# Optimization experiments

Measured on AMD Instinct MI355X. Metric: run time of the kernel, lower is better.

The kernel has to match this reference:

```python
import jax, jax.numpy as jnp
import numpy as np

N = 100000   # nodes
E = 1600000  # edges
IN = 64      # in_channels
H = 128      # hidden_features
G = 1024     # graphs in batch
NUM_REST = 3 # num_layers (extra GraphConv layers)


def setup_inputs() -> dict:
    key = jax.random.key(0)
    ks = jax.random.split(key, 12)
    x = jax.random.normal(ks[0], (N, IN), jnp.float32)
    edge_index = jax.random.randint(ks[1], (2, E), 0, N)
    edge_attr = jax.random.uniform(ks[2], (E,), jnp.float32)
    batch = jnp.sort(jax.random.randint(ks[3], (N,), 0, G))

    def glorot(k, shape, fan_in):
        return jax.random.normal(k, shape, jnp.float32) / np.float32(np.sqrt(fan_in))

    # GraphConv layer 0: in -> hidden (lin_root: no bias, lin_rel: bias)
    W_root0 = glorot(ks[4], (H, IN), IN)
    W_rel0 = glorot(ks[5], (H, IN), IN)
    b0 = jnp.zeros((H,), jnp.float32)
    # GraphConv layers 1..3: hidden -> hidden (stacked)
    W_root_r = glorot(ks[6], (NUM_REST, H, H), H)
    W_rel_r = glorot(ks[7], (NUM_REST, H, H), H)
    b_r = jnp.zeros((NUM_REST, H), jnp.float32)
    # MLPReadout: [H -> H//2 -> 1]
    Wr1 = glorot(ks[8], (H // 2, H), H)
    br1 = jnp.zeros((H // 2,), jnp.float32)
    Wr2 = glorot(ks[9], (1, H // 2), H // 2)
    br2 = jnp.zeros((1,), jnp.float32)
    return dict(x=x, edge_index=edge_index, edge_attr=edge_attr, batch=batch,
                W_root0=W_root0, W_rel0=W_rel0, b0=b0,
                W_root_r=W_root_r, W_rel_r=W_rel_r, b_r=b_r,
                Wr1=Wr1, br1=br1, Wr2=Wr2, br2=br2)


def graph_conv(x, src, dst, ew, W_root, W_rel, b):
    # PyG GraphConv (aggr='add'):
    #   out_i = W_rel @ sum_{j->i} e_ji * x_j + b + W_root @ x_i
    msg = ew[:, None] * x[src]                                   # [E, d]
    agg = jax.ops.segment_sum(msg, dst, num_segments=x.shape[0])  # [N, d]
    return agg @ W_rel.T + b + x @ W_root.T


def reference(x, edge_index, edge_attr, batch,
              W_root0, W_rel0, b0, W_root_r, W_rel_r, b_r,
              Wr1, br1, Wr2, br2):
    src, dst = edge_index[0], edge_index[1]
    y = graph_conv(x, src, dst, edge_attr, W_root0, W_rel0, b0)
    for l in range(W_root_r.shape[0]):
        y = graph_conv(y, src, dst, edge_attr, W_root_r[l], W_rel_r[l], b_r[l])
    # MLPReadout: Linear -> ReLU -> Linear
    y = jax.nn.relu(y @ Wr1.T + br1)
    y = y @ Wr2.T + br2                                           # [N, 1]
    # scatter-mean over graph assignment
    num = jax.ops.segment_sum(y, batch, num_segments=G)           # [G, 1]
    cnt = jax.ops.segment_sum(jnp.ones((y.shape[0], 1), y.dtype), batch,
                              num_segments=G)
    return num / jnp.maximum(cnt, 1.0)                            # [G, 1]
```

## Files before the change

kernel.cpp:

```cpp
#include <hip/hip_runtime.h>
#include <hip/hip_fp16.h>
#include <cstdint>
#include <cstddef>

#define NNODES 100000
#define NEDGES 1600000
#define NGRAPH 1024

#define BK 256
#define NBUCKET 391
#define CHUNK 4096
#define NCHUNK 391
#define NBE (NBUCKET * NCHUNK)

typedef __attribute__((ext_vector_type(8))) short short8;
typedef __attribute__((ext_vector_type(8))) unsigned short ushort8;
typedef __attribute__((ext_vector_type(4))) float f32x4;

__device__ inline float b2f(unsigned short u) {
  return __uint_as_float(((unsigned int)u) << 16);
}
__device__ inline unsigned short f2b(float f) {
  unsigned int x = __float_as_uint(f);
  x += 0x7fffu + ((x >> 16) & 1u);
  return (unsigned short)(x >> 16);
}
__device__ inline unsigned int pack_edge(int src, float w) {
  unsigned short hb = __half_as_ushort(__float2half_rn(w));
  return ((unsigned int)src << 15) | ((unsigned int)hb >> 1);
}
__device__ inline void unpack_edge(unsigned int p, int& src, float& w) {
  src = (int)(p >> 15);
  w = __half2float(__ushort_as_half((unsigned short)((p & 0x7fffu) << 1)));
}

__global__ __launch_bounds__(256) void prepack_kernel(
    const float* __restrict__ Wrel0, const float* __restrict__ Wroot0,
    const float* __restrict__ WrelR, const float* __restrict__ WrootR,
    const float* __restrict__ Wr1, unsigned short* __restrict__ dst)
{
  int g = blockIdx.x * 256 + threadIdx.x;
  if (g >= 15360) return;
  const float* src; int H, K, r; unsigned short* out;
  if (g < 1024)       { src = Wrel0;  H = 128; K = 64;  r = g;        out = dst + r * 8; }
  else if (g < 2048)  { src = Wroot0; H = 128; K = 64;  r = g - 1024; out = dst + 8192 + r * 8; }
  else if (g < 8192)  { int m = g - 2048; int l = m / 2048; r = m % 2048;
                        src = WrelR + l * 16384;  H = 128; K = 128;
                        out = dst + 16384 + l * 16384 + r * 8; }
  else if (g < 14336) { int m = g - 8192; int l = m / 2048; r = m % 2048;
                        src = WrootR + l * 16384; H = 128; K = 128;
                        out = dst + 65536 + l * 16384 + r * 8; }
  else                { src = Wr1;    H = 64;  K = 128; r = g - 14336; out = dst + 114688 + r * 8; }
  int n = r % H, k8 = r / H;
  const float* s = src + (size_t)n * K + k8 * 8;
#pragma unroll
  for (int j = 0; j < 8; j++) out[j] = f2b(s[j]);
}

__global__ __launch_bounds__(256) void cvt_x_kernel(
    const float* __restrict__ x, unsigned short* __restrict__ xb)
{
  int i = blockIdx.x * 256 + threadIdx.x;
  if (i * 4 >= NNODES * 64) return;
  float4 v = *(const float4*)(x + i * 4);
  ushort4 o;
  o.x = f2b(v.x); o.y = f2b(v.y); o.z = f2b(v.z); o.w = f2b(v.w);
  *(ushort4*)(xb + i * 4) = o;
}

__global__ __launch_bounds__(256) void bucket_count_kernel(
    const int* __restrict__ ei, int* __restrict__ cnt)
{
  __shared__ int hist[NBUCKET];
  for (int i = threadIdx.x; i < NBUCKET; i += 256) hist[i] = 0;
  __syncthreads();
  int base = blockIdx.x * CHUNK;
  for (int t = threadIdx.x; t < CHUNK; t += 256) {
    int e = base + t;
    if (e < NEDGES) atomicAdd(&hist[ei[NEDGES + e] >> 8], 1);
  }
  __syncthreads();
  for (int i = threadIdx.x; i < NBUCKET; i += 256)
    cnt[i * NCHUNK + blockIdx.x] = hist[i];
}

__global__ __launch_bounds__(512) void row_scan_kernel(
    int* __restrict__ cnt, int* __restrict__ rowsum)
{
  __shared__ int s[512];
  int b = blockIdx.x, t = threadIdx.x;
  int v = (t < NCHUNK) ? cnt[b * NCHUNK + t] : 0;
  s[t] = v;
  __syncthreads();
#pragma unroll
  for (int off = 1; off < 512; off <<= 1) {
    int u = (t >= off) ? s[t - off] : 0;
    __syncthreads();
    s[t] += u;
    __syncthreads();
  }
  if (t < NCHUNK) cnt[b * NCHUNK + t] = s[t] - v;
  if (t == 511) rowsum[b] = s[511];
}

__global__ __launch_bounds__(512) void rowbase_scan_kernel(
    const int* __restrict__ rowsum, int* __restrict__ rowbase)
{
  __shared__ int s[512];
  int t = threadIdx.x;
  int v = (t < NBUCKET) ? rowsum[t] : 0;
  s[t] = v;
  __syncthreads();
#pragma unroll
  for (int off = 1; off < 512; off <<= 1) {
    int u = (t >= off) ? s[t - off] : 0;
    __syncthreads();
    s[t] += u;
    __syncthreads();
  }
  if (t < NBUCKET) rowbase[t] = s[t] - v;
  if (t == 511) rowbase[NBUCKET] = s[511];
}

__global__ __launch_bounds__(256) void bucket_scatter_kernel(
    const int* __restrict__ ei, const float* __restrict__ ew,
    const int* __restrict__ cnt, const int* __restrict__ rowbase,
    uint2* __restrict__ rec)
{
  __shared__ int pos[NBUCKET];
  for (int i = threadIdx.x; i < NBUCKET; i += 256)
    pos[i] = rowbase[i] + cnt[i * NCHUNK + blockIdx.x];
  __syncthreads();
  int base = blockIdx.x * CHUNK;
  for (int t = threadIdx.x; t < CHUNK; t += 256) {
    int e = base + t;
    if (e < NEDGES) {
      int d = ei[NEDGES + e];
      int p = atomicAdd(&pos[d >> 8], 1);
      rec[p] = make_uint2((unsigned int)d, pack_edge(ei[e], ew[e]));
    }
  }
}

__global__ __launch_bounds__(256) void bucket_fill_kernel(
    const int* __restrict__ rowbase, const uint2* __restrict__ rec,
    unsigned int* __restrict__ epack, int* __restrict__ row_ptr)
{
  __shared__ int off[BK];
  __shared__ int s[256];
  int b = blockIdx.x, t = threadIdx.x;
  int start = rowbase[b];
  int end = rowbase[b + 1];
  int nbase = b * BK;
  off[t] = 0;
  __syncthreads();
  for (int i = start + t; i < end; i += 256)
    atomicAdd(&off[rec[i].x - nbase], 1);
  __syncthreads();
  int v = off[t];
  s[t] = v;
  __syncthreads();
#pragma unroll
  for (int o = 1; o < 256; o <<= 1) {
    int u = (t >= o) ? s[t - o] : 0;
    __syncthreads();
    s[t] += u;
    __syncthreads();
  }
  int ex = s[t] - v;
  int g = nbase + t;
  if (g <= NNODES) row_ptr[g] = start + ex;
  __syncthreads();
  off[t] = ex;
  __syncthreads();
  for (int i = start + t; i < end; i += 256) {
    uint2 r = rec[i];
    int lp = atomicAdd(&off[r.x - nbase], 1);
    epack[start + lp] = r.y;
  }
}

__global__ __launch_bounds__(256) void gptr_kernel(
    const int* __restrict__ batch, int* __restrict__ gptr)
{
  int i = blockIdx.x * 256 + threadIdx.x;
  if (i >= NNODES) return;
  int b = batch[i];
  int bn = (i + 1 < NNODES) ? batch[i + 1] : NGRAPH;
  for (int g = b + 1; g <= bn; g++) gptr[g] = i + 1;
  if (i == 0) for (int g = 0; g <= b; g++) gptr[g] = 0;
}

__global__ __launch_bounds__(256) void agg128_kernel(
    const int* __restrict__ row_ptr, const unsigned int* __restrict__ epack,
    const unsigned short* __restrict__ x, unsigned short* __restrict__ agg)
{
  int node = blockIdx.x * 4 + (threadIdx.x >> 6);
  int lane = threadIdx.x & 63;
  if (node >= NNODES) return;
  int q = lane >> 4, sl = lane & 15;
  int s = row_ptr[node], e = row_ptr[node + 1];
  float acc[8];
#pragma unroll
  for (int j = 0; j < 8; j++) acc[j] = 0.f;

  for (int i = s + q; i < e; i += 16) {
    unsigned int p0 = epack[i];
    unsigned int p1 = (i + 4  < e) ? epack[i + 4]  : 0u;
    unsigned int p2 = (i + 8  < e) ? epack[i + 8]  : 0u;
    unsigned int p3 = (i + 12 < e) ? epack[i + 12] : 0u;
    int s0, s1, s2, s3; float w0, w1, w2, w3;
    unpack_edge(p0, s0, w0);
    unpack_edge(p1, s1, w1);
    unpack_edge(p2, s2, w2);
    unpack_edge(p3, s3, w3);
    ushort8 r0 = *(const ushort8*)(x + (size_t)s0 * 128 + sl * 8);
    ushort8 r1 = *(const ushort8*)(x + (size_t)s1 * 128 + sl * 8);
    ushort8 r2 = *(const ushort8*)(x + (size_t)s2 * 128 + sl * 8);
    ushort8 r3 = *(const ushort8*)(x + (size_t)s3 * 128 + sl * 8);
#pragma unroll
    for (int j = 0; j < 8; j++)
      acc[j] += w0 * b2f(r0[j]) + w1 * b2f(r1[j]) +
                w2 * b2f(r2[j]) + w3 * b2f(r3[j]);
  }
#pragma unroll
  for (int j = 0; j < 8; j++) {
    acc[j] += __shfl_xor(acc[j], 16, 64);
    acc[j] += __shfl_xor(acc[j], 32, 64);
  }
  if (q == 0) {
    ushort8 o;
#pragma unroll
    for (int j = 0; j < 8; j++) o[j] = f2b(acc[j]);
    *(ushort8*)(agg + (size_t)node * 128 + sl * 8) = o;
  }
}

__global__ __launch_bounds__(256) void agg64_kernel(
    const int* __restrict__ row_ptr, const unsigned int* __restrict__ epack,
    const unsigned short* __restrict__ x, unsigned short* __restrict__ agg)
{
  int node = blockIdx.x * 4 + (threadIdx.x >> 6);
  int lane = threadIdx.x & 63;
  if (node >= NNODES) return;
  int q = lane >> 3, sl = lane & 7;
  int s = row_ptr[node], e = row_ptr[node + 1];
  float acc[8];
#pragma unroll
  for (int j = 0; j < 8; j++) acc[j] = 0.f;

  for (int i = s + q; i < e; i += 16) {
    unsigned int p0 = epack[i];
    unsigned int p1 = (i + 8 < e) ? epack[i + 8] : 0u;
    int s0, s1; float w0, w1;
    unpack_edge(p0, s0, w0);
    unpack_edge(p1, s1, w1);
    ushort8 r0 = *(const ushort8*)(x + (size_t)s0 * 64 + sl * 8);
    ushort8 r1 = *(const ushort8*)(x + (size_t)s1 * 64 + sl * 8);
#pragma unroll
    for (int j = 0; j < 8; j++)
      acc[j] += w0 * b2f(r0[j]) + w1 * b2f(r1[j]);
  }
#pragma unroll
  for (int j = 0; j < 8; j++) {
    acc[j] += __shfl_xor(acc[j], 8, 64);
    acc[j] += __shfl_xor(acc[j], 16, 64);
    acc[j] += __shfl_xor(acc[j], 32, 64);
  }
  if (q == 0) {
    ushort8 o;
#pragma unroll
    for (int j = 0; j < 8; j++) o[j] = f2b(acc[j]);
    *(ushort8*)(agg + (size_t)node * 64 + sl * 8) = o;
  }
}

template <int KDIM, int HOUT, int MT, bool DUAL, bool RELU>
__global__ __launch_bounds__(256) void mfma_gemm(
    const unsigned short* __restrict__ A1, const unsigned short* __restrict__ W1,
    const unsigned short* __restrict__ A2, const unsigned short* __restrict__ W2,
    const float* __restrict__ bias, unsigned short* __restrict__ out)
{
  constexpr int NT2 = HOUT / 16;
  constexpr int KC = KDIM / 32;
  const int wave = threadIdx.x >> 6, lane = threadIdx.x & 63;
  const int quad = lane >> 4, l16 = lane & 15;
  const int n0 = (blockIdx.x * 4 + wave) * (MT * 16);

  f32x4 acc[MT][NT2];
#pragma unroll
  for (int m = 0; m < MT; m++)
#pragma unroll
    for (int t = 0; t < NT2; t++) acc[m][t] = (f32x4){0.f, 0.f, 0.f, 0.f};

  int nodes[MT];
#pragma unroll
  for (int m = 0; m < MT; m++) {
    int nd = n0 + m * 16 + l16;
    nodes[m] = nd < NNODES ? nd : NNODES - 1;
  }

#pragma unroll
  for (int c = 0; c < KC; c++) {
    short8 bfr[NT2];
#pragma unroll
    for (int t = 0; t < NT2; t++)
      bfr[t] = *(const short8*)(W1 + ((size_t)(c * 4 + quad) * HOUT + t * 16 + l16) * 8);
#pragma unroll
    for (int m = 0; m < MT; m++) {
      short8 af = *(const short8*)(A1 + (size_t)nodes[m] * KDIM + c * 32 + quad * 8);
#pragma unroll
      for (int t = 0; t < NT2; t++)
        acc[m][t] = __builtin_amdgcn_mfma_f32_16x16x32_bf16(af, bfr[t], acc[m][t], 0, 0, 0);
    }
    if (DUAL) {
#pragma unroll
      for (int t = 0; t < NT2; t++)
        bfr[t] = *(const short8*)(W2 + ((size_t)(c * 4 + quad) * HOUT + t * 16 + l16) * 8);
#pragma unroll
      for (int m = 0; m < MT; m++) {
        short8 af = *(const short8*)(A2 + (size_t)nodes[m] * KDIM + c * 32 + quad * 8);
#pragma unroll
        for (int t = 0; t < NT2; t++)
          acc[m][t] = __builtin_amdgcn_mfma_f32_16x16x32_bf16(af, bfr[t], acc[m][t], 0, 0, 0);
      }
    }
  }

#pragma unroll
  for (int m = 0; m < MT; m++) {
    int rowbase = n0 + m * 16 + quad * 4;
#pragma unroll
    for (int t = 0; t < NT2; t++) {
      float b = bias[t * 16 + l16];
#pragma unroll
      for (int r = 0; r < 4; r++) {
        int nd = rowbase + r;
        if (nd < NNODES) {
          float v = acc[m][t][r] + b;
          if (RELU) v = fmaxf(v, 0.f);
          out[(size_t)nd * HOUT + t * 16 + l16] = f2b(v);
        }
      }
    }
  }
}

__global__ __launch_bounds__(256) void readout_reduce_kernel(
    const unsigned short* __restrict__ h, const float* __restrict__ Wr2,
    const float* __restrict__ br2, const int* __restrict__ gptr,
    float* __restrict__ out)
{
  __shared__ float wsum[4];
  int g = blockIdx.x;
  int s = gptr[g], e = gptr[g + 1];
  int wave = threadIdx.x >> 6, lane = threadIdx.x & 63;
  float w2 = Wr2[lane];
  float acc = 0.f;
  for (int n = s + wave; n < e; n += 4)
    acc += b2f(h[(size_t)n * 64 + lane]) * w2;
#pragma unroll
  for (int off = 32; off >= 1; off >>= 1) acc += __shfl_xor(acc, off, 64);
  if (lane == 0) wsum[wave] = acc;
  __syncthreads();
  if (threadIdx.x == 0) {
    float cnt = (float)(e - s);
    float sum = wsum[0] + wsum[1] + wsum[2] + wsum[3] + cnt * br2[0];
    out[g] = sum / fmaxf(cnt, 1.f);
  }
}

extern "C" void kernel_launch(void* const* d_in, const int* in_sizes, int n_in,
                              void* d_out, int out_size, void* d_ws, size_t ws_size,
                              hipStream_t stream)
{
  const float* x      = (const float*)d_in[0];
  const int*   ei     = (const int*)d_in[1];
  const float* ew     = (const float*)d_in[2];
  const int*   batch  = (const int*)d_in[3];
  const float* Wroot0 = (const float*)d_in[4];
  const float* Wrel0  = (const float*)d_in[5];
  const float* b0     = (const float*)d_in[6];
  const float* WrootR = (const float*)d_in[7];
  const float* WrelR  = (const float*)d_in[8];
  const float* bR     = (const float*)d_in[9];
  const float* Wr1    = (const float*)d_in[10];
  const float* br1    = (const float*)d_in[11];
  const float* Wr2    = (const float*)d_in[12];
  const float* br2    = (const float*)d_in[13];

  char* ws = (char*)d_ws;
  unsigned short* wp   = (unsigned short*)ws;
  unsigned short* xb   = wp + 131072;
  unsigned short* agg0 = xb + (size_t)NNODES * 64;
  unsigned short* bufA = agg0 + (size_t)NNODES * 64;
  unsigned short* bufB = bufA + (size_t)NNODES * 128;
  unsigned short* hbuf = bufB + (size_t)NNODES * 128;
  int*  cnt      = (int*)(hbuf + (size_t)NNODES * 64);
  int*  rowsum   = cnt + ((NBE + 63) & ~63);
  int*  rowbase  = rowsum + NBUCKET + 1;
  int*  row_ptr  = rowbase + NBUCKET + 1;
  int*  gptr     = row_ptr + NNODES + 2;
  unsigned int* epack = (unsigned int*)(gptr + NGRAPH + 2);
  uint2* rec = (uint2*)bufA;

  prepack_kernel<<<60, 256, 0, stream>>>(Wrel0, Wroot0, WrelR, WrootR, Wr1, wp);
  cvt_x_kernel<<<(NNODES * 64 / 4 + 255) / 256, 256, 0, stream>>>(x, xb);

  const unsigned short* pWrel0  = wp;
  const unsigned short* pWroot0 = wp + 8192;
  const unsigned short* pWrelR  = wp + 16384;
  const unsigned short* pWrootR = wp + 65536;
  const unsigned short* pWr1    = wp + 114688;

  bucket_count_kernel<<<NCHUNK, 256, 0, stream>>>(ei, cnt);
  row_scan_kernel<<<NBUCKET, 512, 0, stream>>>(cnt, rowsum);
  rowbase_scan_kernel<<<1, 512, 0, stream>>>(rowsum, rowbase);
  bucket_scatter_kernel<<<NCHUNK, 256, 0, stream>>>(ei, ew, cnt, rowbase, rec);
  bucket_fill_kernel<<<NBUCKET, 256, 0, stream>>>(rowbase, rec, epack, row_ptr);
  gptr_kernel<<<(NNODES + 255) / 256, 256, 0, stream>>>(batch, gptr);

  agg64_kernel<<<(NNODES + 3) / 4, 256, 0, stream>>>(row_ptr, epack, xb, agg0);
  mfma_gemm<64, 128, 2, true, false><<<(NNODES + 127) / 128, 256, 0, stream>>>(
      agg0, pWrel0, xb, pWroot0, b0, bufB);

  unsigned short* bufs[2] = { bufB, bufA };
  for (int l = 0; l < 3; l++) {
    unsigned short* in  = bufs[l & 1];
    unsigned short* agg = bufs[(l & 1) ^ 1];
    agg128_kernel<<<(NNODES + 3) / 4, 256, 0, stream>>>(row_ptr, epack, in, agg);
    mfma_gemm<128, 128, 2, true, false><<<(NNODES + 127) / 128, 256, 0, stream>>>(
        agg, pWrelR + l * 16384, in, pWrootR + l * 16384, bR + l * 128, agg);
  }

  mfma_gemm<128, 64, 4, false, true><<<(NNODES + 255) / 256, 256, 0, stream>>>(
      bufA, pWr1, nullptr, nullptr, br1, hbuf);
  readout_reduce_kernel<<<NGRAPH, 256, 0, stream>>>(hbuf, Wr2, br2, gptr, (float*)d_out);
}
```

Baseline: 506.1 us.

## Fuse neighbor aggregation and dual GEMM into one per-tile layer kernel

Replaces the separate aggregation kernel and dual-input MFMA GEMM with one kernel per layer. Each 64-node tile gathers its neighbor sums into swizzled LDS, then runs the rel/root MFMA GEMMs from LDS and global input. This drops the global write and re-read of the aggregate buffer and one launch per layer. The cost is larger blocks with more serial per-wave work (16 nodes per wave, processed one after another), which may reduce latency hiding for the gather. Output is written as scalar 2-byte stores.

```diff
diff --git a/kernel.cpp b/kernel.cpp
--- a/kernel.cpp
+++ b/kernel.cpp
@@ -191,87 +191,130 @@
   if (i == 0) for (int g = 0; g <= b; g++) gptr[g] = 0;
 }
 
-__global__ __launch_bounds__(256) void agg128_kernel(
+template <int KDIM>
+__global__ __launch_bounds__(256) void fused_layer(
     const int* __restrict__ row_ptr, const unsigned int* __restrict__ epack,
-    const unsigned short* __restrict__ x, unsigned short* __restrict__ agg)
-{
-  int node = blockIdx.x * 4 + (threadIdx.x >> 6);
-  int lane = threadIdx.x & 63;
-  if (node >= NNODES) return;
-  int q = lane >> 4, sl = lane & 15;
-  int s = row_ptr[node], e = row_ptr[node + 1];
-  float acc[8];
-#pragma unroll
-  for (int j = 0; j < 8; j++) acc[j] = 0.f;
-
-  for (int i = s + q; i < e; i += 16) {
-    unsigned int p0 = epack[i];
-    unsigned int p1 = (i + 4  < e) ? epack[i + 4]  : 0u;
-    unsigned int p2 = (i + 8  < e) ? epack[i + 8]  : 0u;
-    unsigned int p3 = (i + 12 < e) ? epack[i + 12] : 0u;
-    int s0, s1, s2, s3; float w0, w1, w2, w3;
-    unpack_edge(p0, s0, w0);
-    unpack_edge(p1, s1, w1);
-    unpack_edge(p2, s2, w2);
-    unpack_edge(p3, s3, w3);
-    ushort8 r0 = *(const ushort8*)(x + (size_t)s0 * 128 + sl * 8);
-    ushort8 r1 = *(const ushort8*)(x + (size_t)s1 * 128 + sl * 8);
-    ushort8 r2 = *(const ushort8*)(x + (size_t)s2 * 128 + sl * 8);
-    ushort8 r3 = *(const ushort8*)(x + (size_t)s3 * 128 + sl * 8);
-#pragma unroll
-    for (int j = 0; j < 8; j++)
-      acc[j] += w0 * b2f(r0[j]) + w1 * b2f(r1[j]) +
-                w2 * b2f(r2[j]) + w3 * b2f(r3[j]);
-  }
-#pragma unroll
-  for (int j = 0; j < 8; j++) {
-    acc[j] += __shfl_xor(acc[j], 16, 64);
-    acc[j] += __shfl_xor(acc[j], 32, 64);
-  }
-  if (q == 0) {
-    ushort8 o;
-#pragma unroll
-    for (int j = 0; j < 8; j++) o[j] = f2b(acc[j]);
-    *(ushort8*)(agg + (size_t)node * 128 + sl * 8) = o;
-  }
-}
-
-__global__ __launch_bounds__(256) void agg64_kernel(
-    const int* __restrict__ row_ptr, const unsigned int* __restrict__ epack,
-    const unsigned short* __restrict__ x, unsigned short* __restrict__ agg)
-{
-  int node = blockIdx.x * 4 + (threadIdx.x >> 6);
-  int lane = threadIdx.x & 63;
-  if (node >= NNODES) return;
-  int q = lane >> 3, sl = lane & 7;
-  int s = row_ptr[node], e = row_ptr[node + 1];
-  float acc[8];
-#pragma unroll
-  for (int j = 0; j < 8; j++) acc[j] = 0.f;
-
-  for (int i = s + q; i < e; i += 16) {
-    unsigned int p0 = epack[i];
-    unsigned int p1 = (i + 8 < e) ? epack[i + 8] : 0u;
-    int s0, s1; float w0, w1;
-    unpack_edge(p0, s0, w0);
-    unpack_edge(p1, s1, w1);
-    ushort8 r0 = *(const ushort8*)(x + (size_t)s0 * 64 + sl * 8);
-    ushort8 r1 = *(const ushort8*)(x + (size_t)s1 * 64 + sl * 8);
-#pragma unroll
-    for (int j = 0; j < 8; j++)
-      acc[j] += w0 * b2f(r0[j]) + w1 * b2f(r1[j]);
-  }
-#pragma unroll
-  for (int j = 0; j < 8; j++) {
-    acc[j] += __shfl_xor(acc[j], 8, 64);
-    acc[j] += __shfl_xor(acc[j], 16, 64);
-    acc[j] += __shfl_xor(acc[j], 32, 64);
-  }
-  if (q == 0) {
-    ushort8 o;
-#pragma unroll
-    for (int j = 0; j < 8; j++) o[j] = f2b(acc[j]);
-    *(ushort8*)(agg + (size_t)node * 64 + sl * 8) = o;
+    const unsigned short* __restrict__ in,
+    const unsigned short* __restrict__ W1, const unsigned short* __restrict__ W2,
+    const float* __restrict__ bias, unsigned short* __restrict__ out)
+{
+  constexpr int ROWB = KDIM * 2;
+  __shared__ __align__(16) unsigned char lds[64 * ROWB];
+  const int wave = threadIdx.x >> 6, lane = threadIdx.x & 63;
+  const int tile0 = blockIdx.x * 64;
+
+  {
+    int q, sl;
+    if (KDIM == 128) { q = lane >> 4; sl = lane & 15; }
+    else             { q = lane >> 3; sl = lane & 7;  }
+    for (int nn = 0; nn < 16; nn++) {
+      int lrow = wave * 16 + nn;
+      int node = tile0 + lrow;
+      float acc[8];
+#pragma unroll
+      for (int j = 0; j < 8; j++) acc[j] = 0.f;
+      if (node < NNODES) {
+        int s = row_ptr[node], e = row_ptr[node + 1];
+        if (KDIM == 128) {
+          for (int i = s + q; i < e; i += 16) {
+            unsigned int p0 = epack[i];
+            unsigned int p1 = (i + 4  < e) ? epack[i + 4]  : 0u;
+            unsigned int p2 = (i + 8  < e) ? epack[i + 8]  : 0u;
+            unsigned int p3 = (i + 12 < e) ? epack[i + 12] : 0u;
+            int s0, s1, s2, s3; float w0, w1, w2, w3;
+            unpack_edge(p0, s0, w0);
+            unpack_edge(p1, s1, w1);
+            unpack_edge(p2, s2, w2);
+            unpack_edge(p3, s3, w3);
+            ushort8 r0 = *(const ushort8*)(in + (size_t)s0 * 128 + sl * 8);
+            ushort8 r1 = *(const ushort8*)(in + (size_t)s1 * 128 + sl * 8);
+            ushort8 r2 = *(const ushort8*)(in + (size_t)s2 * 128 + sl * 8);
+            ushort8 r3 = *(const ushort8*)(in + (size_t)s3 * 128 + sl * 8);
+#pragma unroll
+            for (int j = 0; j < 8; j++)
+              acc[j] += w0 * b2f(r0[j]) + w1 * b2f(r1[j]) +
+                        w2 * b2f(r2[j]) + w3 * b2f(r3[j]);
+          }
+#pragma unroll
+          for (int j = 0; j < 8; j++) {
+            acc[j] += __shfl_xor(acc[j], 16, 64);
+            acc[j] += __shfl_xor(acc[j], 32, 64);
+          }
+        } else {
+          for (int i = s + q; i < e; i += 16) {
+            unsigned int p0 = epack[i];
+            unsigned int p1 = (i + 8 < e) ? epack[i + 8] : 0u;
+            int s0, s1; float w0, w1;
+            unpack_edge(p0, s0, w0);
+            unpack_edge(p1, s1, w1);
+            ushort8 r0 = *(const ushort8*)(in + (size_t)s0 * 64 + sl * 8);
+            ushort8 r1 = *(const ushort8*)(in + (size_t)s1 * 64 + sl * 8);
+#pragma unroll
+            for (int j = 0; j < 8; j++)
+              acc[j] += w0 * b2f(r0[j]) + w1 * b2f(r1[j]);
+          }
+#pragma unroll
+          for (int j = 0; j < 8; j++) {
+            acc[j] += __shfl_xor(acc[j], 8, 64);
+            acc[j] += __shfl_xor(acc[j], 16, 64);
+            acc[j] += __shfl_xor(acc[j], 32, 64);
+          }
+        }
+      }
+      if (q == 0) {
+        ushort8 o;
+#pragma unroll
+        for (int j = 0; j < 8; j++) o[j] = f2b(acc[j]);
+        int boff = lrow * ROWB + ((sl * 16) ^ ((lrow & 7) << 4));
+        *(ushort8*)(lds + boff) = o;
+      }
+    }
+  }
+  __syncthreads();
+
+  constexpr int NT2 = 8;
+  constexpr int KC = KDIM / 32;
+  const int quad = lane >> 4, l16 = lane & 15;
+  const int lrow = wave * 16 + l16;
+  int gnode = tile0 + lrow; if (gnode >= NNODES) gnode = NNODES - 1;
+  const unsigned short* inrow = in + (size_t)gnode * KDIM;
+
+  f32x4 acc2[NT2];
+#pragma unroll
+  for (int t = 0; t < NT2; t++) acc2[t] = (f32x4){0.f, 0.f, 0.f, 0.f};
+
+#pragma unroll
+  for (int c = 0; c < KC; c++) {
+    short8 bfr[NT2];
+#pragma unroll
+    for (int t = 0; t < NT2; t++)
+      bfr[t] = *(const short8*)(W1 + ((size_t)(c * 4 + quad) * 128 + t * 16 + l16) * 8);
+    int boff = lrow * ROWB + (((c * 32 + quad * 8) * 2) ^ ((lrow & 7) << 4));
+    short8 af1 = *(const short8*)(lds + boff);
+#pragma unroll
+    for (int t = 0; t < NT2; t++)
+      acc2[t] = __builtin_amdgcn_mfma_f32_16x16x32_bf16(af1, bfr[t], acc2[t], 0, 0, 0);
+#pragma unroll
+    for (int t = 0; t < NT2; t++)
+      bfr[t] = *(const short8*)(W2 + ((size_t)(c * 4 + quad) * 128 + t * 16 + l16) * 8);
+    short8 af2 = *(const short8*)(inrow + c * 32 + quad * 8);
+#pragma unroll
+    for (int t = 0; t < NT2; t++)
+      acc2[t] = __builtin_amdgcn_mfma_f32_16x16x32_bf16(af2, bfr[t], acc2[t], 0, 0, 0);
+  }
+
+  int rowbase = tile0 + wave * 16 + quad * 4;
+#pragma unroll
+  for (int t = 0; t < NT2; t++) {
+    float b = bias[t * 16 + l16];
+#pragma unroll
+    for (int r = 0; r < 4; r++) {
+      int nd = rowbase + r;
+      if (nd < NNODES) {
+        float v = acc2[t][r] + b;
+        out[(size_t)nd * 128 + t * 16 + l16] = f2b(v);
+      }
+    }
   }
 }
 
@@ -420,17 +463,17 @@
   bucket_fill_kernel<<<NBUCKET, 256, 0, stream>>>(rowbase, rec, epack, row_ptr);
   gptr_kernel<<<(NNODES + 255) / 256, 256, 0, stream>>>(batch, gptr);
 
-  agg64_kernel<<<(NNODES + 3) / 4, 256, 0, stream>>>(row_ptr, epack, xb, agg0);
-  mfma_gemm<64, 128, 2, true, false><<<(NNODES + 127) / 128, 256, 0, stream>>>(
-      agg0, pWrel0, xb, pWroot0, b0, bufB);
+  const int NTILE = (NNODES + 63) / 64;
+
+  fused_layer<64><<<NTILE, 256, 0, stream>>>(
+      row_ptr, epack, xb, pWrel0, pWroot0, b0, bufB);
 
   unsigned short* bufs[2] = { bufB, bufA };
   for (int l = 0; l < 3; l++) {
     unsigned short* in  = bufs[l & 1];
-    unsigned short* agg = bufs[(l & 1) ^ 1];
-    agg128_kernel<<<(NNODES + 3) / 4, 256, 0, stream>>>(row_ptr, epack, in, agg);
-    mfma_gemm<128, 128, 2, true, false><<<(NNODES + 127) / 128, 256, 0, stream>>>(
-        agg, pWrelR + l * 16384, in, pWrootR + l * 16384, bR + l * 128, agg);
+    unsigned short* out = bufs[(l & 1) ^ 1];
+    fused_layer<128><<<NTILE, 256, 0, stream>>>(
+        row_ptr, epack, in, pWrelR + l * 16384, pWrootR + l * 16384, bR + l * 128, out);
   }
 
   mfma_gemm<128, 64, 4, false, true><<<(NNODES + 255) / 256, 256, 0, stream>>>(
```

Measured after the change: 548.2 us. 1.08x slower.

## Process two nodes per wave in aggregation and fuse readout MLP with graph pooling

Applied to the files above, without the earlier changes.

The aggregation kernels now have each wave handle two destination nodes at once, interleaving their edge loads to raise memory-level parallelism, and launch half as many blocks. The readout GEMM, ReLU, second linear layer and per-graph sum are fused into one MFMA kernel that atomically adds per-node scalars into a per-graph buffer, followed by a tiny finalize kernel. This removes the hidden-activation round trip through memory and the separate reduce pass. The costs are extra register pressure, wasted lanes when the two nodes' degrees differ, float atomic contention on sorted batch ids, and nondeterministic summation order.

```diff
diff --git a/kernel.cpp b/kernel.cpp
--- a/kernel.cpp
+++ b/kernel.cpp
@@ -195,44 +195,66 @@
     const int* __restrict__ row_ptr, const unsigned int* __restrict__ epack,
     const unsigned short* __restrict__ x, unsigned short* __restrict__ agg)
 {
-  int node = blockIdx.x * 4 + (threadIdx.x >> 6);
+  int pair = blockIdx.x * 4 + (threadIdx.x >> 6);
+  int nodeA = pair * 2, nodeB = pair * 2 + 1;
   int lane = threadIdx.x & 63;
-  if (node >= NNODES) return;
+  if (nodeA >= NNODES) return;
   int q = lane >> 4, sl = lane & 15;
-  int s = row_ptr[node], e = row_ptr[node + 1];
-  float acc[8];
-#pragma unroll
-  for (int j = 0; j < 8; j++) acc[j] = 0.f;
-
-  for (int i = s + q; i < e; i += 16) {
-    unsigned int p0 = epack[i];
-    unsigned int p1 = (i + 4  < e) ? epack[i + 4]  : 0u;
-    unsigned int p2 = (i + 8  < e) ? epack[i + 8]  : 0u;
-    unsigned int p3 = (i + 12 < e) ? epack[i + 12] : 0u;
-    int s0, s1, s2, s3; float w0, w1, w2, w3;
-    unpack_edge(p0, s0, w0);
-    unpack_edge(p1, s1, w1);
-    unpack_edge(p2, s2, w2);
-    unpack_edge(p3, s3, w3);
-    ushort8 r0 = *(const ushort8*)(x + (size_t)s0 * 128 + sl * 8);
-    ushort8 r1 = *(const ushort8*)(x + (size_t)s1 * 128 + sl * 8);
-    ushort8 r2 = *(const ushort8*)(x + (size_t)s2 * 128 + sl * 8);
-    ushort8 r3 = *(const ushort8*)(x + (size_t)s3 * 128 + sl * 8);
-#pragma unroll
-    for (int j = 0; j < 8; j++)
-      acc[j] += w0 * b2f(r0[j]) + w1 * b2f(r1[j]) +
-                w2 * b2f(r2[j]) + w3 * b2f(r3[j]);
+  int sA = row_ptr[nodeA], eA = row_ptr[nodeA + 1];
+  int sB = eA, eB = eA;
+  if (nodeB < NNODES) eB = row_ptr[nodeB + 1];
+  float accA[8], accB[8];
+#pragma unroll
+  for (int j = 0; j < 8; j++) { accA[j] = 0.f; accB[j] = 0.f; }
+
+  for (int iA = sA + q, iB = sB + q; iA < eA || iB < eB; iA += 16, iB += 16) {
+    unsigned int a0 = (iA      < eA) ? epack[iA]      : 0u;
+    unsigned int a1 = (iA + 4  < eA) ? epack[iA + 4]  : 0u;
+    unsigned int a2 = (iA + 8  < eA) ? epack[iA + 8]  : 0u;
+    unsigned int a3 = (iA + 12 < eA) ? epack[iA + 12] : 0u;
+    unsigned int b0 = (iB      < eB) ? epack[iB]      : 0u;
+    unsigned int b1 = (iB + 4  < eB) ? epack[iB + 4]  : 0u;
+    unsigned int b2 = (iB + 8  < eB) ? epack[iB + 8]  : 0u;
+    unsigned int b3 = (iB + 12 < eB) ? epack[iB + 12] : 0u;
+    int sa0, sa1, sa2, sa3, sb0, sb1, sb2, sb3;
+    float wa0, wa1, wa2, wa3, wb0, wb1, wb2, wb3;
+    unpack_edge(a0, sa0, wa0); unpack_edge(a1, sa1, wa1);
+    unpack_edge(a2, sa2, wa2); unpack_edge(a3, sa3, wa3);
+    unpack_edge(b0, sb0, wb0); unpack_edge(b1, sb1, wb1);
+    unpack_edge(b2, sb2, wb2); unpack_edge(b3, sb3, wb3);
+    ushort8 rA0 = *(const ushort8*)(x + (size_t)sa0 * 128 + sl * 8);
+    ushort8 rA1 = *(const ushort8*)(x + (size_t)sa1 * 128 + sl * 8);
+    ushort8 rA2 = *(const ushort8*)(x + (size_t)sa2 * 128 + sl * 8);
+    ushort8 rA3 = *(const ushort8*)(x + (size_t)sa3 * 128 + sl * 8);
+    ushort8 rB0 = *(const ushort8*)(x + (size_t)sb0 * 128 + sl * 8);
+    ushort8 rB1 = *(const ushort8*)(x + (size_t)sb1 * 128 + sl * 8);
+    ushort8 rB2 = *(const ushort8*)(x + (size_t)sb2 * 128 + sl * 8);
+    ushort8 rB3 = *(const ushort8*)(x + (size_t)sb3 * 128 + sl * 8);
+#pragma unroll
+    for (int j = 0; j < 8; j++) {
+      accA[j] += wa0 * b2f(rA0[j]) + wa1 * b2f(rA1[j]) +
+                 wa2 * b2f(rA2[j]) + wa3 * b2f(rA3[j]);
+      accB[j] += wb0 * b2f(rB0[j]) + wb1 * b2f(rB1[j]) +
+                 wb2 * b2f(rB2[j]) + wb3 * b2f(rB3[j]);
+    }
   }
 #pragma unroll
   for (int j = 0; j < 8; j++) {
-    acc[j] += __shfl_xor(acc[j], 16, 64);
-    acc[j] += __shfl_xor(acc[j], 32, 64);
+    accA[j] += __shfl_xor(accA[j], 16, 64);
+    accA[j] += __shfl_xor(accA[j], 32, 64);
+    accB[j] += __shfl_xor(accB[j], 16, 64);
+    accB[j] += __shfl_xor(accB[j], 32, 64);
   }
   if (q == 0) {
     ushort8 o;
 #pragma unroll
-    for (int j = 0; j < 8; j++) o[j] = f2b(acc[j]);
-    *(ushort8*)(agg + (size_t)node * 128 + sl * 8) = o;
+    for (int j = 0; j < 8; j++) o[j] = f2b(accA[j]);
+    *(ushort8*)(agg + (size_t)nodeA * 128 + sl * 8) = o;
+  } else if (q == 1 && nodeB < NNODES) {
+    ushort8 o;
+#pragma unroll
+    for (int j = 0; j < 8; j++) o[j] = f2b(accB[j]);
+    *(ushort8*)(agg + (size_t)nodeB * 128 + sl * 8) = o;
   }
 }
 
@@ -240,38 +262,55 @@
     const int* __restrict__ row_ptr, const unsigned int* __restrict__ epack,
     const unsigned short* __restrict__ x, unsigned short* __restrict__ agg)
 {
-  int node = blockIdx.x * 4 + (threadIdx.x >> 6);
+  int pair = blockIdx.x * 4 + (threadIdx.x >> 6);
+  int nodeA = pair * 2, nodeB = pair * 2 + 1;
   int lane = threadIdx.x & 63;
-  if (node >= NNODES) return;
+  if (nodeA >= NNODES) return;
   int q = lane >> 3, sl = lane & 7;
-  int s = row_ptr[node], e = row_ptr[node + 1];
-  float acc[8];
-#pragma unroll
-  for (int j = 0; j < 8; j++) acc[j] = 0.f;
-
-  for (int i = s + q; i < e; i += 16) {
-    unsigned int p0 = epack[i];
-    unsigned int p1 = (i + 8 < e) ? epack[i + 8] : 0u;
-    int s0, s1; float w0, w1;
-    unpack_edge(p0, s0, w0);
-    unpack_edge(p1, s1, w1);
-    ushort8 r0 = *(const ushort8*)(x + (size_t)s0 * 64 + sl * 8);
-    ushort8 r1 = *(const ushort8*)(x + (size_t)s1 * 64 + sl * 8);
-#pragma unroll
-    for (int j = 0; j < 8; j++)
-      acc[j] += w0 * b2f(r0[j]) + w1 * b2f(r1[j]);
+  int sA = row_ptr[nodeA], eA = row_ptr[nodeA + 1];
+  int sB = eA, eB = eA;
+  if (nodeB < NNODES) eB = row_ptr[nodeB + 1];
+  float accA[8], accB[8];
+#pragma unroll
+  for (int j = 0; j < 8; j++) { accA[j] = 0.f; accB[j] = 0.f; }
+
+  for (int iA = sA + q, iB = sB + q; iA < eA || iB < eB; iA += 16, iB += 16) {
+    unsigned int a0 = (iA     < eA) ? epack[iA]     : 0u;
+    unsigned int a1 = (iA + 8 < eA) ? epack[iA + 8] : 0u;
+    unsigned int b0 = (iB     < eB) ? epack[iB]     : 0u;
+    unsigned int b1 = (iB + 8 < eB) ? epack[iB + 8] : 0u;
+    int sa0, sa1, sb0, sb1; float wa0, wa1, wb0, wb1;
+    unpack_edge(a0, sa0, wa0); unpack_edge(a1, sa1, wa1);
+    unpack_edge(b0, sb0, wb0); unpack_edge(b1, sb1, wb1);
+    ushort8 rA0 = *(const ushort8*)(x + (size_t)sa0 * 64 + sl * 8);
+    ushort8 rA1 = *(const ushort8*)(x + (size_t)sa1 * 64 + sl * 8);
+    ushort8 rB0 = *(const ushort8*)(x + (size_t)sb0 * 64 + sl * 8);
+    ushort8 rB1 = *(const ushort8*)(x + (size_t)sb1 * 64 + sl * 8);
+#pragma unroll
+    for (int j = 0; j < 8; j++) {
+      accA[j] += wa0 * b2f(rA0[j]) + wa1 * b2f(rA1[j]);
+      accB[j] += wb0 * b2f(rB0[j]) + wb1 * b2f(rB1[j]);
+    }
   }
 #pragma unroll
   for (int j = 0; j < 8; j++) {
-    acc[j] += __shfl_xor(acc[j], 8, 64);
-    acc[j] += __shfl_xor(acc[j], 16, 64);
-    acc[j] += __shfl_xor(acc[j], 32, 64);
+    accA[j] += __shfl_xor(accA[j], 8, 64);
+    accA[j] += __shfl_xor(accA[j], 16, 64);
+    accA[j] += __shfl_xor(accA[j], 32, 64);
+    accB[j] += __shfl_xor(accB[j], 8, 64);
+    accB[j] += __shfl_xor(accB[j], 16, 64);
+    accB[j] += __shfl_xor(accB[j], 32, 64);
   }
   if (q == 0) {
     ushort8 o;
 #pragma unroll
-    for (int j = 0; j < 8; j++) o[j] = f2b(acc[j]);
-    *(ushort8*)(agg + (size_t)node * 64 + sl * 8) = o;
+    for (int j = 0; j < 8; j++) o[j] = f2b(accA[j]);
+    *(ushort8*)(agg + (size_t)nodeA * 64 + sl * 8) = o;
+  } else if (q == 1 && nodeB < NNODES) {
+    ushort8 o;
+#pragma unroll
+    for (int j = 0; j < 8; j++) o[j] = f2b(accB[j]);
+    *(ushort8*)(agg + (size_t)nodeB * 64 + sl * 8) = o;
   }
 }
 
@@ -346,28 +385,78 @@
   }
 }
 
-__global__ __launch_bounds__(256) void readout_reduce_kernel(
-    const unsigned short* __restrict__ h, const float* __restrict__ Wr2,
-    const float* __restrict__ br2, const int* __restrict__ gptr,
-    float* __restrict__ out)
-{
-  __shared__ float wsum[4];
-  int g = blockIdx.x;
-  int s = gptr[g], e = gptr[g + 1];
-  int wave = threadIdx.x >> 6, lane = threadIdx.x & 63;
-  float w2 = Wr2[lane];
-  float acc = 0.f;
-  for (int n = s + wave; n < e; n += 4)
-    acc += b2f(h[(size_t)n * 64 + lane]) * w2;
-#pragma unroll
-  for (int off = 32; off >= 1; off >>= 1) acc += __shfl_xor(acc, off, 64);
-  if (lane == 0) wsum[wave] = acc;
-  __syncthreads();
-  if (threadIdx.x == 0) {
-    float cnt = (float)(e - s);
-    float sum = wsum[0] + wsum[1] + wsum[2] + wsum[3] + cnt * br2[0];
-    out[g] = sum / fmaxf(cnt, 1.f);
-  }
+__global__ __launch_bounds__(256) void readout_fused_kernel(
+    const unsigned short* __restrict__ A1, const unsigned short* __restrict__ W1,
+    const float* __restrict__ br1, const float* __restrict__ Wr2,
+    const int* __restrict__ batch, float* __restrict__ gnum)
+{
+  constexpr int NT2 = 4, KC = 4, MT = 4;
+  const int wave = threadIdx.x >> 6, lane = threadIdx.x & 63;
+  const int quad = lane >> 4, l16 = lane & 15;
+  const int n0 = (blockIdx.x * 4 + wave) * (MT * 16);
+
+  f32x4 acc[MT][NT2];
+#pragma unroll
+  for (int m = 0; m < MT; m++)
+#pragma unroll
+    for (int t = 0; t < NT2; t++) acc[m][t] = (f32x4){0.f, 0.f, 0.f, 0.f};
+
+  int nodes[MT];
+#pragma unroll
+  for (int m = 0; m < MT; m++) {
+    int nd = n0 + m * 16 + l16;
+    nodes[m] = nd < NNODES ? nd : NNODES - 1;
+  }
+
+#pragma unroll
+  for (int c = 0; c < KC; c++) {
+    short8 bfr[NT2];
+#pragma unroll
+    for (int t = 0; t < NT2; t++)
+      bfr[t] = *(const short8*)(W1 + ((size_t)(c * 4 + quad) * 64 + t * 16 + l16) * 8);
+#pragma unroll
+    for (int m = 0; m < MT; m++) {
+      short8 af = *(const short8*)(A1 + (size_t)nodes[m] * 128 + c * 32 + quad * 8);
+#pragma unroll
+      for (int t = 0; t < NT2; t++)
+        acc[m][t] = __builtin_amdgcn_mfma_f32_16x16x32_bf16(af, bfr[t], acc[m][t], 0, 0, 0);
+    }
+  }
+
+  float bv[NT2], wv[NT2];
+#pragma unroll
+  for (int t = 0; t < NT2; t++) {
+    bv[t] = br1[t * 16 + l16];
+    wv[t] = Wr2[t * 16 + l16];
+  }
+#pragma unroll
+  for (int m = 0; m < MT; m++) {
+    int rowbase = n0 + m * 16 + quad * 4;
+#pragma unroll
+    for (int r = 0; r < 4; r++) {
+      float p = 0.f;
+#pragma unroll
+      for (int t = 0; t < NT2; t++)
+        p += fmaxf(acc[m][t][r] + bv[t], 0.f) * wv[t];
+      p += __shfl_xor(p, 1, 64);
+      p += __shfl_xor(p, 2, 64);
+      p += __shfl_xor(p, 4, 64);
+      p += __shfl_xor(p, 8, 64);
+      int nd = rowbase + r;
+      if (l16 == 0 && nd < NNODES)
+        atomicAdd(&gnum[batch[nd]], p);
+    }
+  }
+}
+
+__global__ __launch_bounds__(256) void finalize_kernel(
+    const float* __restrict__ gnum, const int* __restrict__ gptr,
+    const float* __restrict__ br2, float* __restrict__ out)
+{
+  int g = blockIdx.x * 256 + threadIdx.x;
+  if (g >= NGRAPH) return;
+  float cnt = (float)(gptr[g + 1] - gptr[g]);
+  out[g] = (gnum[g] + cnt * br2[0]) / fmaxf(cnt, 1.f);
 }
 
 extern "C" void kernel_launch(void* const* d_in, const int* in_sizes, int n_in,
@@ -403,9 +492,11 @@
   int*  gptr     = row_ptr + NNODES + 2;
   unsigned int* epack = (unsigned int*)(gptr + NGRAPH + 2);
   uint2* rec = (uint2*)bufA;
+  float* gnum = (float*)hbuf;
 
   prepack_kernel<<<60, 256, 0, stream>>>(Wrel0, Wroot0, WrelR, WrootR, Wr1, wp);
   cvt_x_kernel<<<(NNODES * 64 / 4 + 255) / 256, 256, 0, stream>>>(x, xb);
+  hipMemsetAsync(gnum, 0, NGRAPH * sizeof(float), stream);
 
   const unsigned short* pWrel0  = wp;
   const unsigned short* pWroot0 = wp + 8192;
@@ -420,7 +511,7 @@
   bucket_fill_kernel<<<NBUCKET, 256, 0, stream>>>(rowbase, rec, epack, row_ptr);
   gptr_kernel<<<(NNODES + 255) / 256, 256, 0, stream>>>(batch, gptr);
 
-  agg64_kernel<<<(NNODES + 3) / 4, 256, 0, stream>>>(row_ptr, epack, xb, agg0);
+  agg64_kernel<<<(NNODES + 7) / 8, 256, 0, stream>>>(row_ptr, epack, xb, agg0);
   mfma_gemm<64, 128, 2, true, false><<<(NNODES + 127) / 128, 256, 0, stream>>>(
       agg0, pWrel0, xb, pWroot0, b0, bufB);
 
@@ -428,12 +519,12 @@
   for (int l = 0; l < 3; l++) {
     unsigned short* in  = bufs[l & 1];
     unsigned short* agg = bufs[(l & 1) ^ 1];
-    agg128_kernel<<<(NNODES + 3) / 4, 256, 0, stream>>>(row_ptr, epack, in, agg);
+    agg128_kernel<<<(NNODES + 7) / 8, 256, 0, stream>>>(row_ptr, epack, in, agg);
     mfma_gemm<128, 128, 2, true, false><<<(NNODES + 127) / 128, 256, 0, stream>>>(
         agg, pWrelR + l * 16384, in, pWrootR + l * 16384, bR + l * 128, agg);
   }
 
-  mfma_gemm<128, 64, 4, false, true><<<(NNODES + 255) / 256, 256, 0, stream>>>(
-      bufA, pWr1, nullptr, nullptr, br1, hbuf);
-  readout_reduce_kernel<<<NGRAPH, 256, 0, stream>>>(hbuf, Wr2, br2, gptr, (float*)d_out);
-}
+  readout_fused_kernel<<<(NNODES + 255) / 256, 256, 0, stream>>>(
+      bufA, pWr1, br1, Wr2, batch, gnum);
+  finalize_kernel<<<(NGRAPH + 255) / 256, 256, 0, stream>>>(gnum, gptr, br2, (float*)d_out);
+}
```

Measured after the change: 524.0 us. 3.5% more time.

## Split node aggregation across two waves and fuse readout MLP with graph pooling

Applied to the files above, without the earlier changes.

The aggregation kernels now give each node two waves, each covering alternate 16-edge strides, and combine their partial sums through shared memory. The goal is more parallelism per node and more loads in flight for the edge gathers. Separately, the readout Linear+ReLU GEMM is fused with the second Linear and the per-graph sum, using atomics into a per-graph accumulator followed by a small finalize kernel. This removes the hbuf write and re-read, at the cost of float atomics that make the summation order nondeterministic.

```diff
diff --git a/kernel.cpp b/kernel.cpp
--- a/kernel.cpp
+++ b/kernel.cpp
@@ -195,16 +195,17 @@
     const int* __restrict__ row_ptr, const unsigned int* __restrict__ epack,
     const unsigned short* __restrict__ x, unsigned short* __restrict__ agg)
 {
-  int node = blockIdx.x * 4 + (threadIdx.x >> 6);
-  int lane = threadIdx.x & 63;
-  if (node >= NNODES) return;
-  int q = lane >> 4, sl = lane & 15;
+  __shared__ float part[4][128];
+  const int wave = threadIdx.x >> 6, lane = threadIdx.x & 63;
+  const int node = blockIdx.x * 2 + (wave >> 1);
+  const int half = wave & 1;
+  const int q = lane >> 4, sl = lane & 15;
   int s = row_ptr[node], e = row_ptr[node + 1];
   float acc[8];
 #pragma unroll
   for (int j = 0; j < 8; j++) acc[j] = 0.f;
 
-  for (int i = s + q; i < e; i += 16) {
+  for (int i = s + half * 16 + q; i < e; i += 32) {
     unsigned int p0 = epack[i];
     unsigned int p1 = (i + 4  < e) ? epack[i + 4]  : 0u;
     unsigned int p2 = (i + 8  < e) ? epack[i + 8]  : 0u;
@@ -229,9 +230,15 @@
     acc[j] += __shfl_xor(acc[j], 32, 64);
   }
   if (q == 0) {
+#pragma unroll
+    for (int j = 0; j < 8; j++) part[wave][sl * 8 + j] = acc[j];
+  }
+  __syncthreads();
+  if (half == 0 && q == 0) {
     ushort8 o;
 #pragma unroll
-    for (int j = 0; j < 8; j++) o[j] = f2b(acc[j]);
+    for (int j = 0; j < 8; j++)
+      o[j] = f2b(part[wave][sl * 8 + j] + part[wave + 1][sl * 8 + j]);
     *(ushort8*)(agg + (size_t)node * 128 + sl * 8) = o;
   }
 }
@@ -240,16 +247,17 @@
     const int* __restrict__ row_ptr, const unsigned int* __restrict__ epack,
     const unsigned short* __restrict__ x, unsigned short* __restrict__ agg)
 {
-  int node = blockIdx.x * 4 + (threadIdx.x >> 6);
-  int lane = threadIdx.x & 63;
-  if (node >= NNODES) return;
-  int q = lane >> 3, sl = lane & 7;
+  __shared__ float part[4][64];
+  const int wave = threadIdx.x >> 6, lane = threadIdx.x & 63;
+  const int node = blockIdx.x * 2 + (wave >> 1);
+  const int half = wave & 1;
+  const int q = lane >> 3, sl = lane & 7;
   int s = row_ptr[node], e = row_ptr[node + 1];
   float acc[8];
 #pragma unroll
   for (int j = 0; j < 8; j++) acc[j] = 0.f;
 
-  for (int i = s + q; i < e; i += 16) {
+  for (int i = s + half * 16 + q; i < e; i += 32) {
     unsigned int p0 = epack[i];
     unsigned int p1 = (i + 8 < e) ? epack[i + 8] : 0u;
     int s0, s1; float w0, w1;
@@ -268,9 +276,15 @@
     acc[j] += __shfl_xor(acc[j], 32, 64);
   }
   if (q == 0) {
+#pragma unroll
+    for (int j = 0; j < 8; j++) part[wave][sl * 8 + j] = acc[j];
+  }
+  __syncthreads();
+  if (half == 0 && q == 0) {
     ushort8 o;
 #pragma unroll
-    for (int j = 0; j < 8; j++) o[j] = f2b(acc[j]);
+    for (int j = 0; j < 8; j++)
+      o[j] = f2b(part[wave][sl * 8 + j] + part[wave + 1][sl * 8 + j]);
     *(ushort8*)(agg + (size_t)node * 64 + sl * 8) = o;
   }
 }
@@ -346,28 +360,78 @@
   }
 }
 
-__global__ __launch_bounds__(256) void readout_reduce_kernel(
-    const unsigned short* __restrict__ h, const float* __restrict__ Wr2,
-    const float* __restrict__ br2, const int* __restrict__ gptr,
-    float* __restrict__ out)
-{
-  __shared__ float wsum[4];
-  int g = blockIdx.x;
-  int s = gptr[g], e = gptr[g + 1];
-  int wave = threadIdx.x >> 6, lane = threadIdx.x & 63;
-  float w2 = Wr2[lane];
-  float acc = 0.f;
-  for (int n = s + wave; n < e; n += 4)
-    acc += b2f(h[(size_t)n * 64 + lane]) * w2;
-#pragma unroll
-  for (int off = 32; off >= 1; off >>= 1) acc += __shfl_xor(acc, off, 64);
-  if (lane == 0) wsum[wave] = acc;
-  __syncthreads();
-  if (threadIdx.x == 0) {
-    float cnt = (float)(e - s);
-    float sum = wsum[0] + wsum[1] + wsum[2] + wsum[3] + cnt * br2[0];
-    out[g] = sum / fmaxf(cnt, 1.f);
-  }
+__global__ __launch_bounds__(256) void readout_fused_kernel(
+    const unsigned short* __restrict__ A1, const unsigned short* __restrict__ W1,
+    const float* __restrict__ br1, const float* __restrict__ Wr2,
+    const int* __restrict__ batch, float* __restrict__ gnum)
+{
+  constexpr int NT2 = 4, KC = 4, MT = 4;
+  const int wave = threadIdx.x >> 6, lane = threadIdx.x & 63;
+  const int quad = lane >> 4, l16 = lane & 15;
+  const int n0 = (blockIdx.x * 4 + wave) * (MT * 16);
+
+  f32x4 acc[MT][NT2];
+#pragma unroll
+  for (int m = 0; m < MT; m++)
+#pragma unroll
+    for (int t = 0; t < NT2; t++) acc[m][t] = (f32x4){0.f, 0.f, 0.f, 0.f};
+
+  int nodes[MT];
+#pragma unroll
+  for (int m = 0; m < MT; m++) {
+    int nd = n0 + m * 16 + l16;
+    nodes[m] = nd < NNODES ? nd : NNODES - 1;
+  }
+
+#pragma unroll
+  for (int c = 0; c < KC; c++) {
+    short8 bfr[NT2];
+#pragma unroll
+    for (int t = 0; t < NT2; t++)
+      bfr[t] = *(const short8*)(W1 + ((size_t)(c * 4 + quad) * 64 + t * 16 + l16) * 8);
+#pragma unroll
+    for (int m = 0; m < MT; m++) {
+      short8 af = *(const short8*)(A1 + (size_t)nodes[m] * 128 + c * 32 + quad * 8);
+#pragma unroll
+      for (int t = 0; t < NT2; t++)
+        acc[m][t] = __builtin_amdgcn_mfma_f32_16x16x32_bf16(af, bfr[t], acc[m][t], 0, 0, 0);
+    }
+  }
+
+  float bv[NT2], wv[NT2];
+#pragma unroll
+  for (int t = 0; t < NT2; t++) {
+    bv[t] = br1[t * 16 + l16];
+    wv[t] = Wr2[t * 16 + l16];
+  }
+#pragma unroll
+  for (int m = 0; m < MT; m++) {
+    int rowbase = n0 + m * 16 + quad * 4;
+#pragma unroll
+    for (int r = 0; r < 4; r++) {
+      float p = 0.f;
+#pragma unroll
+      for (int t = 0; t < NT2; t++)
+        p += fmaxf(acc[m][t][r] + bv[t], 0.f) * wv[t];
+      p += __shfl_xor(p, 1, 64);
+      p += __shfl_xor(p, 2, 64);
+      p += __shfl_xor(p, 4, 64);
+      p += __shfl_xor(p, 8, 64);
+      int nd = rowbase + r;
+      if (l16 == 0 && nd < NNODES)
+        atomicAdd(&gnum[batch[nd]], p);
+    }
+  }
+}
+
+__global__ __launch_bounds__(256) void finalize_kernel(
+    const float* __restrict__ gnum, const int* __restrict__ gptr,
+    const float* __restrict__ br2, float* __restrict__ out)
+{
+  int g = blockIdx.x * 256 + threadIdx.x;
+  if (g >= NGRAPH) return;
+  float cnt = (float)(gptr[g + 1] - gptr[g]);
+  out[g] = (gnum[g] + cnt * br2[0]) / fmaxf(cnt, 1.f);
 }
 
 extern "C" void kernel_launch(void* const* d_in, const int* in_sizes, int n_in,
@@ -403,9 +467,11 @@
   int*  gptr     = row_ptr + NNODES + 2;
   unsigned int* epack = (unsigned int*)(gptr + NGRAPH + 2);
   uint2* rec = (uint2*)bufA;
+  float* gnum = (float*)hbuf;
 
   prepack_kernel<<<60, 256, 0, stream>>>(Wrel0, Wroot0, WrelR, WrootR, Wr1, wp);
   cvt_x_kernel<<<(NNODES * 64 / 4 + 255) / 256, 256, 0, stream>>>(x, xb);
+  hipMemsetAsync(gnum, 0, NGRAPH * sizeof(float), stream);
 
   const unsigned short* pWrel0  = wp;
   const unsigned short* pWroot0 = wp + 8192;
@@ -420,7 +486,7 @@
   bucket_fill_kernel<<<NBUCKET, 256, 0, stream>>>(rowbase, rec, epack, row_ptr);
   gptr_kernel<<<(NNODES + 255) / 256, 256, 0, stream>>>(batch, gptr);
 
-  agg64_kernel<<<(NNODES + 3) / 4, 256, 0, stream>>>(row_ptr, epack, xb, agg0);
+  agg64_kernel<<<NNODES / 2, 256, 0, stream>>>(row_ptr, epack, xb, agg0);
   mfma_gemm<64, 128, 2, true, false><<<(NNODES + 127) / 128, 256, 0, stream>>>(
       agg0, pWrel0, xb, pWroot0, b0, bufB);
 
@@ -428,12 +494,12 @@
   for (int l = 0; l < 3; l++) {
     unsigned short* in  = bufs[l & 1];
     unsigned short* agg = bufs[(l & 1) ^ 1];
-    agg128_kernel<<<(NNODES + 3) / 4, 256, 0, stream>>>(row_ptr, epack, in, agg);
+    agg128_kernel<<<NNODES / 2, 256, 0, stream>>>(row_ptr, epack, in, agg);
     mfma_gemm<128, 128, 2, true, false><<<(NNODES + 127) / 128, 256, 0, stream>>>(
         agg, pWrelR + l * 16384, in, pWrootR + l * 16384, bR + l * 128, agg);
   }
 
-  mfma_gemm<128, 64, 4, false, true><<<(NNODES + 255) / 256, 256, 0, stream>>>(
-      bufA, pWr1, nullptr, nullptr, br1, hbuf);
-  readout_reduce_kernel<<<NGRAPH, 256, 0, stream>>>(hbuf, Wr2, br2, gptr, (float*)d_out);
-}
+  readout_fused_kernel<<<(NNODES + 255) / 256, 256, 0, stream>>>(
+      bufA, pWr1, br1, Wr2, batch, gnum);
+  finalize_kernel<<<(NGRAPH + 255) / 256, 256, 0, stream>>>(gnum, gptr, br2, (float*)d_out);
+}
```

After: 589.0 us. 16.4% more time.
